# Optimization experiments

Measured on AMD Instinct MI355X. Metric: run time of the kernel, lower is better.

## Reference

```python
import jax, jax.numpy as jnp
import numpy as np

OUTPUT_SIZE = (7, 7)
SPATIAL_SCALE = 0.0625
B, C, H, W = 4, 256, 38, 38
N_ROIS = 512
IMG = int(W / SPATIAL_SCALE)  # 608


def setup_inputs() -> dict:
    key = jax.random.key(0)
    k_feat, k_bidx, k_xy = jax.random.split(key, 3)
    features = jax.random.normal(k_feat, (B, C, H, W), dtype=jnp.float32)
    batch_idx = jax.random.randint(k_bidx, (N_ROIS, 1), 0, B).astype(jnp.float32)
    # (x1,x2) and (y1,y2) sampled in image coords, sorted so x1<=x2, y1<=y2
    xy = jax.random.uniform(k_xy, (N_ROIS, 2, 2), minval=0.0, maxval=float(IMG))
    xy = jnp.sort(xy, axis=2)  # [N, {x,y}, {lo,hi}]
    rois = jnp.concatenate(
        [batch_idx, xy[:, 0, 0:1], xy[:, 1, 0:1], xy[:, 0, 1:2], xy[:, 1, 1:2]],
        axis=1,
    ).astype(jnp.float32)  # [N,5] = (b, x1, y1, x2, y2)
    return {"features": features, "rois": rois}


def _roi_pool(features, rois, output_size, spatial_scale):
    Ph, Pw = output_size
    Bf, Cf, Hf, Wf = features.shape
    bidx = rois[:, 0].astype(jnp.int32)
    # torch .long() truncates toward zero; coords are non-negative here
    coords = jnp.trunc(rois[:, 1:5] * spatial_scale).astype(jnp.int32)
    x1 = jnp.clip(coords[:, 0], 0, Wf - 1)
    y1 = jnp.clip(coords[:, 1], 0, Hf - 1)
    x2 = jnp.clip(coords[:, 2], 0, Wf - 1)
    y2 = jnp.clip(coords[:, 3], 0, Hf - 1)
    hh = y2 - y1 + 1  # region height (inclusive slice y1:y2+1)
    ww = x2 - x1 + 1
    feat = features[bidx]  # [N,C,H,W] per-ROI gathered feature map
    hs = jnp.arange(Hf)
    ws = jnp.arange(Wf)
    NEG = jnp.finfo(features.dtype).min
    # adaptive_max_pool2d bins: start = floor(p*size/P), end = ceil((p+1)*size/P)
    # 2D max over a rectangle = max over rows then max over cols.
    rows = []
    for p in range(Ph):
        s = y1 + (p * hh) // Ph
        e = y1 + ((p + 1) * hh + Ph - 1) // Ph  # ceil div
        m = (hs[None, :] >= s[:, None]) & (hs[None, :] < e[:, None])  # [N,H]
        rows.append(jnp.max(jnp.where(m[:, None, :, None], feat, NEG), axis=2))  # [N,C,W]
    ry = jnp.stack(rows, axis=2)  # [N,C,Ph,W]
    cols = []
    for q in range(Pw):
        s = x1 + (q * ww) // Pw
        e = x1 + ((q + 1) * ww + Pw - 1) // Pw
        m = (ws[None, :] >= s[:, None]) & (ws[None, :] < e[:, None])  # [N,W]
        cols.append(jnp.max(jnp.where(m[:, None, None, :], ry, NEG), axis=3))  # [N,C,Ph]
    return jnp.stack(cols, axis=3)  # [N,C,Ph,Pw]


def reference(features, rois):
    return _roi_pool(features, rois, OUTPUT_SIZE, SPATIAL_SCALE)
```

## Files before the change

kernel.cpp:

```cpp
#include <hip/hip_runtime.h>


#define NROIS 512
#define CCH   256
#define FH    38
#define FW    38
#define HW    (FH * FW)
#define SCALE 0.0625f
#define NEGF  (-3.402823466e+38f)

#define FEATT_BYTES ((size_t)4 * HW * CCH * sizeof(float))

__global__ __launch_bounds__(256) void transpose_bucket_kernel(
    const float* __restrict__ src, const float* __restrict__ rois,
    float* __restrict__ dst, int* __restrict__ perm,
    int* __restrict__ cntG, int* __restrict__ offG)
{
    __shared__ float tile[4][257];
    __shared__ int cntS[4], baseS[4];

    const int b  = blockIdx.y;
    const int s0 = blockIdx.x * 4;
    const int t  = threadIdx.x;

    const float4 v = *(const float4*)(src + ((size_t)(b * CCH + t)) * HW + s0);
    tile[0][t] = v.x; tile[1][t] = v.y; tile[2][t] = v.z; tile[3][t] = v.w;
    __syncthreads();

    const int s = t >> 6;
    const int m = t & 63;
    float* drow = dst + ((size_t)b * HW + s0 + s) * CCH;
    #pragma unroll
    for (int k = 0; k < 4; ++k)
        drow[m + 64 * k] = tile[s][m + 64 * k];

    if (blockIdx.x == 0 && blockIdx.y == 0) {
        if (t < 4) cntS[t] = 0;
        __syncthreads();
        const int b0 = (int)rois[t * 5];
        const int p0 = atomicAdd(&cntS[b0], 1);
        const int b1 = (int)rois[(t + 256) * 5];
        const int p1 = atomicAdd(&cntS[b1], 1);
        __syncthreads();
        if (t == 0) {
            int acc = 0;
            #pragma unroll
            for (int i = 0; i < 4; ++i) {
                baseS[i] = acc;
                cntG[i] = cntS[i];
                offG[i] = acc;
                acc += cntS[i];
            }
        }
        __syncthreads();
        perm[baseS[b0] + p0] = t;
        perm[baseS[b1] + p1] = t + 256;
    }
}

template <int WW>
__device__ __forceinline__ void pool_one(
    const float* __restrict__ rb, int h, float (&acc)[7])
{
    for (int y = 0; y < h; ++y) {
        float v[WW];
        #pragma unroll
        for (int j = 0; j < WW; ++j) v[j] = rb[j * CCH];
        #pragma unroll
        for (int q = 0; q < 7; ++q) {
            const int xs = (q * WW) / 7;
            const int xe = ((q + 1) * WW + 6) / 7;
            #pragma unroll
            for (int j = xs; j < xe; ++j)
                acc[q] = fmaxf(acc[q], v[j]);
        }
        rb += (size_t)FW * CCH;
    }
}

template <int NB>
__device__ __forceinline__ void write_out(
    float* __restrict__ outb, const float (*__restrict__ sm)[65], int tid)
{
    #pragma unroll
    for (int flat = 0; flat < 64 * NB; flat += 256) {
        const int f = flat + tid;
        if (f < 64 * NB) {
            const int c = f / NB;
            const int l = f - c * NB;
            outb[c * 49 + l] = sm[l][c];
        }
    }
}

__global__ __launch_bounds__(256) void roipool_kernel(
    const float* __restrict__ featT,
    const float* __restrict__ rois,
    const int* __restrict__ perm,
    const int* __restrict__ cntG,
    const int* __restrict__ offG,
    float* __restrict__ out)
{
    __shared__ float smem[28][65];

    const int bid  = blockIdx.x;
    const int xcd  = bid & 7;
    const int slot = bid >> 3;
    const int img  = xcd >> 1;
    const int half = xcd & 1;
    const int tid  = threadIdx.x;
    const int wv   = __builtin_amdgcn_readfirstlane(tid >> 6);
    const int lane = tid & 63;

    const int cnt = cntG[img];
    const int off = offG[img];
    const int nunits = cnt * 8;

    for (int g = slot * 2 + half; g < nunits; g += 1024) {
        const int r  = perm[off + (g >> 3)];
        const int u  = g & 7;
        const int cg = u & 3;
        const int ph = u >> 2;

        const float* rr = rois + r * 5;
        const int bb = (int)rr[0];
        int x1 = (int)(rr[1] * SCALE);
        int y1 = (int)(rr[2] * SCALE);
        int x2 = (int)(rr[3] * SCALE);
        int y2 = (int)(rr[4] * SCALE);
        x1 = min(max(x1, 0), FW - 1);
        y1 = min(max(y1, 0), FH - 1);
        x2 = min(max(x2, 0), FW - 1);
        y2 = min(max(y2, 0), FH - 1);
        const int hh = y2 - y1 + 1;
        const int ww = x2 - x1 + 1;

        const int p = 4 * ph + wv;
        if (p < 7) {
            const int ys = y1 + (p * hh) / 7;
            const int h  = (y1 + ((p + 1) * hh + 6) / 7) - ys;

            const float* rb0 = featT + (size_t)bb * HW * CCH + cg * 64 + lane
                             + (size_t)(ys * FW + x1) * CCH;

            float acc[7];
            #pragma unroll
            for (int q = 0; q < 7; ++q) acc[q] = NEGF;

            switch (ww) {
                case  1: pool_one< 1>(rb0, h, acc); break;
                case  2: pool_one< 2>(rb0, h, acc); break;
                case  3: pool_one< 3>(rb0, h, acc); break;
                case  4: pool_one< 4>(rb0, h, acc); break;
                case  5: pool_one< 5>(rb0, h, acc); break;
                case  6: pool_one< 6>(rb0, h, acc); break;
                case  7: pool_one< 7>(rb0, h, acc); break;
                case  8: pool_one< 8>(rb0, h, acc); break;
                case  9: pool_one< 9>(rb0, h, acc); break;
                case 10: pool_one<10>(rb0, h, acc); break;
                case 11: pool_one<11>(rb0, h, acc); break;
                case 12: pool_one<12>(rb0, h, acc); break;
                case 13: pool_one<13>(rb0, h, acc); break;
                case 14: pool_one<14>(rb0, h, acc); break;
                case 15: pool_one<15>(rb0, h, acc); break;
                case 16: pool_one<16>(rb0, h, acc); break;
                case 17: pool_one<17>(rb0, h, acc); break;
                case 18: pool_one<18>(rb0, h, acc); break;
                case 19: pool_one<19>(rb0, h, acc); break;
                case 20: pool_one<20>(rb0, h, acc); break;
                case 21: pool_one<21>(rb0, h, acc); break;
                case 22: pool_one<22>(rb0, h, acc); break;
                case 23: pool_one<23>(rb0, h, acc); break;
                case 24: pool_one<24>(rb0, h, acc); break;
                case 25: pool_one<25>(rb0, h, acc); break;
                case 26: pool_one<26>(rb0, h, acc); break;
                case 27: pool_one<27>(rb0, h, acc); break;
                case 28: pool_one<28>(rb0, h, acc); break;
                case 29: pool_one<29>(rb0, h, acc); break;
                case 30: pool_one<30>(rb0, h, acc); break;
                case 31: pool_one<31>(rb0, h, acc); break;
                case 32: pool_one<32>(rb0, h, acc); break;
                case 33: pool_one<33>(rb0, h, acc); break;
                case 34: pool_one<34>(rb0, h, acc); break;
                case 35: pool_one<35>(rb0, h, acc); break;
                case 36: pool_one<36>(rb0, h, acc); break;
                case 37: pool_one<37>(rb0, h, acc); break;
                default: pool_one<38>(rb0, h, acc); break;
            }

            #pragma unroll
            for (int q = 0; q < 7; ++q)
                smem[wv * 7 + q][lane] = acc[q];
        }
        __syncthreads();

        float* outb = out + (size_t)r * (CCH * 49) + cg * (64 * 49) + ph * 28;
        if (ph == 0) write_out<28>(outb, smem, tid);
        else         write_out<21>(outb, smem, tid);
        __syncthreads();
    }
}

__global__ __launch_bounds__(256) void roipool_fallback(
    const float* __restrict__ feat,
    const float* __restrict__ rois,
    float* __restrict__ out)
{
    int idx = blockIdx.x * blockDim.x + threadIdx.x;
    int q = idx % 7;
    int t = idx / 7;
    int p = t % 7;
    t /= 7;
    int c = t % CCH;
    int n = t / CCH;

    const float* r = rois + n * 5;
    int b  = (int)r[0];
    int x1 = (int)(r[1] * SCALE);
    int y1 = (int)(r[2] * SCALE);
    int x2 = (int)(r[3] * SCALE);
    int y2 = (int)(r[4] * SCALE);
    x1 = min(max(x1, 0), FW - 1);
    y1 = min(max(y1, 0), FH - 1);
    x2 = min(max(x2, 0), FW - 1);
    y2 = min(max(y2, 0), FH - 1);
    int hh = y2 - y1 + 1, ww = x2 - x1 + 1;

    int ys = y1 + (p * hh) / 7, ye = y1 + ((p + 1) * hh + 6) / 7;
    int xs = x1 + (q * ww) / 7, xe = x1 + ((q + 1) * ww + 6) / 7;

    const float* base = feat + ((size_t)b * CCH + c) * HW;
    float m = NEGF;
    for (int y = ys; y < ye; ++y)
        for (int x = xs; x < xe; ++x)
            m = fmaxf(m, base[y * FW + x]);
    out[idx] = m;
}

extern "C" void kernel_launch(void* const* d_in, const int* in_sizes, int n_in,
                              void* d_out, int out_size, void* d_ws, size_t ws_size,
                              hipStream_t stream) {
    const float* feat = (const float*)d_in[0];
    const float* rois = (const float*)d_in[1];
    float* out = (float*)d_out;

    const size_t need = FEATT_BYTES + (NROIS + 8) * sizeof(int);
    if (ws_size < need) {
        const int total = NROIS * CCH * 49;
        roipool_fallback<<<(total + 255) / 256, 256, 0, stream>>>(feat, rois, out);
        return;
    }

    float* featT = (float*)d_ws;
    int*   perm  = (int*)((char*)d_ws + FEATT_BYTES);
    int*   cntG  = perm + NROIS;
    int*   offG  = cntG + 4;

    dim3 tg(HW / 4, 4);
    transpose_bucket_kernel<<<tg, 256, 0, stream>>>(feat, rois, featT,
                                                    perm, cntG, offG);

    roipool_kernel<<<4096, 256, 0, stream>>>(featT, rois, perm, cntG, offG, out);
}
```

Baseline: 30.32 us.

## Sort ROIs by height descending and use atomic work queue for dynamic scheduling

Replaces the per-image bucketing and the static XCD-aware grid-stride schedule with a counting sort of ROIs by region height, largest first, plus a global atomic work-queue counter. Blocks fetch work units dynamically in longest-first order. The aim is better load balance across ROIs of very different sizes, at the cost of losing per-image L2/XCD locality and paying one atomic plus a barrier per unit. The grid shrinks from 4096 blocks to 1024 persistent blocks.

```diff
diff --git a/kernel.cpp b/kernel.cpp
--- a/kernel.cpp
+++ b/kernel.cpp
@@ -8,16 +8,25 @@
 #define HW    (FH * FW)
 #define SCALE 0.0625f
 #define NEGF  (-3.402823466e+38f)
+#define NUNITS (NROIS * 8)
 
 #define FEATT_BYTES ((size_t)4 * HW * CCH * sizeof(float))
 
-__global__ __launch_bounds__(256) void transpose_bucket_kernel(
+__device__ __forceinline__ int roi_hh(const float* __restrict__ rr)
+{
+    int y1 = (int)(rr[2] * SCALE);
+    int y2 = (int)(rr[4] * SCALE);
+    y1 = min(max(y1, 0), FH - 1);
+    y2 = min(max(y2, 0), FH - 1);
+    return y2 - y1 + 1;
+}
+
+__global__ __launch_bounds__(256) void transpose_sort_kernel(
     const float* __restrict__ src, const float* __restrict__ rois,
-    float* __restrict__ dst, int* __restrict__ perm,
-    int* __restrict__ cntG, int* __restrict__ offG)
+    float* __restrict__ dst, int* __restrict__ perm, int* __restrict__ qhead)
 {
     __shared__ float tile[4][257];
-    __shared__ int cntS[4], baseS[4];
+    __shared__ int hist[40];
 
     const int b  = blockIdx.y;
     const int s0 = blockIdx.x * 4;
@@ -35,26 +44,25 @@
         drow[m + 64 * k] = tile[s][m + 64 * k];
 
     if (blockIdx.x == 0 && blockIdx.y == 0) {
-        if (t < 4) cntS[t] = 0;
-        __syncthreads();
-        const int b0 = (int)rois[t * 5];
-        const int p0 = atomicAdd(&cntS[b0], 1);
-        const int b1 = (int)rois[(t + 256) * 5];
-        const int p1 = atomicAdd(&cntS[b1], 1);
+        if (t < 40) hist[t] = 0;
+        __syncthreads();
+        const int h0 = roi_hh(rois + t * 5);
+        const int h1 = roi_hh(rois + (t + 256) * 5);
+        atomicAdd(&hist[h0], 1);
+        atomicAdd(&hist[h1], 1);
         __syncthreads();
         if (t == 0) {
             int acc = 0;
-            #pragma unroll
-            for (int i = 0; i < 4; ++i) {
-                baseS[i] = acc;
-                cntG[i] = cntS[i];
-                offG[i] = acc;
-                acc += cntS[i];
+            for (int h = 38; h >= 1; --h) {
+                const int c = hist[h];
+                hist[h] = acc;
+                acc += c;
             }
-        }
-        __syncthreads();
-        perm[baseS[b0] + p0] = t;
-        perm[baseS[b1] + p1] = t + 256;
+            *qhead = 0;
+        }
+        __syncthreads();
+        perm[atomicAdd(&hist[h0], 1)] = t;
+        perm[atomicAdd(&hist[h1], 1)] = t + 256;
     }
 }
 
@@ -97,30 +105,25 @@
     const float* __restrict__ featT,
     const float* __restrict__ rois,
     const int* __restrict__ perm,
-    const int* __restrict__ cntG,
-    const int* __restrict__ offG,
+    int* __restrict__ qhead,
     float* __restrict__ out)
 {
     __shared__ float smem[28][65];
-
-    const int bid  = blockIdx.x;
-    const int xcd  = bid & 7;
-    const int slot = bid >> 3;
-    const int img  = xcd >> 1;
-    const int half = xcd & 1;
+    __shared__ int sQ;
+
     const int tid  = threadIdx.x;
     const int wv   = __builtin_amdgcn_readfirstlane(tid >> 6);
     const int lane = tid & 63;
 
-    const int cnt = cntG[img];
-    const int off = offG[img];
-    const int nunits = cnt * 8;
-
-    for (int g = slot * 2 + half; g < nunits; g += 1024) {
-        const int r  = perm[off + (g >> 3)];
-        const int u  = g & 7;
-        const int cg = u & 3;
-        const int ph = u >> 2;
+    for (;;) {
+        if (tid == 0) sQ = atomicAdd(qhead, 1);
+        __syncthreads();
+        const int g = sQ;
+        if (g >= NUNITS) break;
+
+        const int r  = perm[g >> 3];
+        const int cg = g & 3;
+        const int ph = (g >> 2) & 1;
 
         const float* rr = rois + r * 5;
         const int bb = (int)rr[0];
@@ -244,7 +247,7 @@
     const float* rois = (const float*)d_in[1];
     float* out = (float*)d_out;
 
-    const size_t need = FEATT_BYTES + (NROIS + 8) * sizeof(int);
+    const size_t need = FEATT_BYTES + (NROIS + 1) * sizeof(int);
     if (ws_size < need) {
         const int total = NROIS * CCH * 49;
         roipool_fallback<<<(total + 255) / 256, 256, 0, stream>>>(feat, rois, out);
@@ -253,12 +256,10 @@
 
     float* featT = (float*)d_ws;
     int*   perm  = (int*)((char*)d_ws + FEATT_BYTES);
-    int*   cntG  = perm + NROIS;
-    int*   offG  = cntG + 4;
+    int*   qhead = perm + NROIS;
 
     dim3 tg(HW / 4, 4);
-    transpose_bucket_kernel<<<tg, 256, 0, stream>>>(feat, rois, featT,
-                                                    perm, cntG, offG);
-
-    roipool_kernel<<<4096, 256, 0, stream>>>(featT, rois, perm, cntG, offG, out);
-}
+    transpose_sort_kernel<<<tg, 256, 0, stream>>>(feat, rois, featT, perm, qhead);
+
+    roipool_kernel<<<1024, 256, 0, stream>>>(featT, rois, perm, qhead, out);
+}
```

New measurement: 77.27 us. 2.55x slower.
